# Performance work log

Measured on AMD Instinct MI355X. Metric: run time of the kernel, lower is better.

## Reference

```python
import jax, jax.numpy as jnp
import numpy as np

DIAG_MASK = 1e20  # value added on the diagonal to exclude self as negative


def setup_inputs() -> dict:
    key = jax.random.key(0)
    k1, k2, k3 = jax.random.split(key, 3)
    B, D_in, D_out = 4096, 1024, 1024
    anchor_x = jax.random.normal(k1, (B, D_in), dtype=jnp.float32)
    pos_x = jax.random.normal(k2, (B, D_in), dtype=jnp.float32)
    W = jax.random.normal(k3, (D_in, D_out), dtype=jnp.float32) * (1.0 / np.sqrt(D_in))
    b = jnp.zeros((D_out,), dtype=jnp.float32)
    return {"anchor_x": anchor_x, "pos_x": pos_x, "W": W, "b": b}


def reference(anchor_x, pos_x, W, b):
    # Encoder: simple dense projection (stand-in for the wrapped BERT encoder).
    anchor = anchor_x @ W + b          # [B, D]
    pos = pos_x @ W + b                # [B, D]

    # Pairwise squared distances dist[i,j] = ||anchor_i - pos_j||^2,
    # computed via the GEMM identity |a|^2 + |p|^2 - 2 a.p (same math as the
    # original broadcasted (a_i - p_j)^2 reduce_sum, far less memory traffic).
    a2 = jnp.sum(anchor * anchor, axis=-1, keepdims=True)       # [B, 1]
    p2 = jnp.sum(pos * pos, axis=-1, keepdims=True).T           # [1, B]
    dist = a2 + p2 - 2.0 * (anchor @ pos.T)                     # [B, B]

    B = dist.shape[0]
    mask_dist = dist + jnp.eye(B, dtype=dist.dtype) * DIAG_MASK  # mask diagonal
    indices = jnp.argmin(mask_dist, axis=-1)                     # [B] hard negatives
    neg = pos[indices]                                           # gather [B, D]

    return jnp.concatenate([anchor, pos, neg], axis=-1)          # [B, 3D]
```

## Files before the change

### kernel.cpp

```cpp
#include <hip/hip_runtime.h>


typedef short s8v __attribute__((ext_vector_type(8)));
typedef _Float16 h8v __attribute__((ext_vector_type(8)));
typedef float f4v __attribute__((ext_vector_type(4)));
typedef unsigned short u16;

#define B  4096
#define D  1024
#define OLD 3072
#define OLD16 6144
#define LDK 68

__device__ __forceinline__ u16 f2bf(float f) {
  union { float f; unsigned u; } v; v.f = f;
  unsigned r = v.u + 0x7FFFu + ((v.u >> 16) & 1u);
  return (u16)(r >> 16);
}
__device__ __forceinline__ float bf2f(u16 s) {
  union { unsigned u; float f; } v; v.u = ((unsigned)s) << 16;
  return v.f;
}

__device__ __forceinline__ void gld16(const void* g, void* l) {
  __builtin_amdgcn_global_load_lds(
      (const __attribute__((address_space(1))) unsigned int*)g,
      (__attribute__((address_space(3))) unsigned int*)l, 16, 0, 0);
}

__device__ __forceinline__ unsigned ldsaddr(const void* p) {
  const __attribute__((address_space(3))) char* lp =
      (const __attribute__((address_space(3))) char*)p;
  unsigned a;
  __builtin_memcpy(&a, &lp, 4);
  return a;
}

struct Top2 { float v1, v2; int j1, j2; };
__device__ __forceinline__ void t2_insert(Top2& t, float v, int j) {
  if (v < t.v1 || (v == t.v1 && j < t.j1)) {
    t.v2 = t.v1; t.j2 = t.j1; t.v1 = v; t.j1 = j;
  } else if (v < t.v2 || (v == t.v2 && j < t.j2)) {
    t.v2 = v; t.j2 = j;
  }
}
struct Top4 { float v[4]; int j[4]; };
__device__ __forceinline__ void t4_insert(Top4& t, float v, int j) {
  if (v < t.v[3] || (v == t.v[3] && j < t.j[3])) {
    int p = 3;
#pragma unroll
    for (int s = 0; s < 3; ++s) {
      if (p > 0 && (v < t.v[p - 1] || (v == t.v[p - 1] && j < t.j[p - 1]))) {
        t.v[p] = t.v[p - 1]; t.j[p] = t.j[p - 1]; --p;
      }
    }
    t.v[p] = v; t.j[p] = j;
  }
}

__global__ void splitT_W(const float* __restrict__ W, u16* __restrict__ WtQ) {
  __shared__ float tile[32][33];
  const int bx = blockIdx.x * 32, by = blockIdx.y * 32;
  const int tx = threadIdx.x, ty = threadIdx.y;
  for (int dy = 0; dy < 32; dy += 8)
    tile[ty + dy][tx] = W[(size_t)(by + ty + dy) * D + bx + tx];
  __syncthreads();
  for (int dy = 0; dy < 32; dy += 8) {
    const float v = tile[tx][ty + dy];
    const u16 h = f2bf(v);
    const size_t o = (size_t)(bx + ty + dy) * 2048 + by + tx;
    WtQ[o] = h;
    WtQ[o + 1024] = f2bf(v - bf2f(h));
  }
}

__global__ __launch_bounds__(256) void splitX2(
    const float* __restrict__ A, const float* __restrict__ P,
    u16* __restrict__ O16, u16* __restrict__ posXq) {
  const int r = blockIdx.x, t = threadIdx.x;
  const bool isPos = r >= B;
  const int row = isPos ? r - B : r;
  const float4 v = *(const float4*)&(isPos ? P : A)[(size_t)row * D + t * 4];
  const float vv[4] = {v.x, v.y, v.z, v.w};
  ushort4 hi, mi;
  u16* hp = &hi.x; u16* mp = &mi.x;
#pragma unroll
  for (int i = 0; i < 4; ++i) {
    hp[i] = f2bf(vv[i]);
    mp[i] = f2bf(vv[i] - bf2f(hp[i]));
  }
  if (isPos) {
    *(ushort4*)&posXq[(size_t)row * 2048 + t * 4] = hi;
    *(ushort4*)&posXq[(size_t)row * 2048 + 1024 + t * 4] = mi;
  } else {
    *(ushort4*)&O16[(size_t)row * OLD16 + 4096 + t * 4] = hi;
    *(ushort4*)&O16[(size_t)row * OLD16 + 5120 + t * 4] = mi;
  }
}

__global__ __launch_bounds__(256) void enc_mfma(
    float* out, const u16* __restrict__ posXq, const u16* __restrict__ WtQ,
    const float* __restrict__ bias, _Float16* __restrict__ Aq,
    _Float16* __restrict__ Pq) {
  __shared__ __align__(16) u16 lAh[4][128 * 32], lAm[4][128 * 32];
  __shared__ __align__(16) u16 lBh[4][128 * 32], lBm[4][128 * 32];
  const u16* O16 = (const u16*)out;
  const int tid = threadIdx.x, lane = tid & 63, wave = tid >> 6;
  const int waveM = wave >> 1, waveN = wave & 1;
  const int row16 = lane & 15, quad = lane >> 4;
  const int g = blockIdx.x + (blockIdx.y << 3);
  const int bx = (g >> 3) & 7;
  const int by = (g & 7) | ((g >> 6) << 3);
  const bool isPos = by >= 32;
  const int Mbase = (by & 31) * 128;
  const int Nbase = bx * 128;
  f4v acc[4][4] = {};
  const int slot = (quad ^ ((row16 >> 1) & 3)) * 8;

  auto STAGE = [&](int buf, int kk) {
#pragma unroll
    for (int i = 0; i < 2; ++i) {
      const int c = i * 256 + tid;
      const int row = c >> 2;
      const int col8 = ((c & 3) ^ ((row >> 1) & 3)) * 8;
      const int lo = (i * 256 + wave * 64) * 8;
      if (isPos) {
        gld16(&posXq[(size_t)(Mbase + row) * 2048 + kk + col8], &lAh[buf][lo]);
        gld16(&posXq[(size_t)(Mbase + row) * 2048 + 1024 + kk + col8], &lAm[buf][lo]);
      } else {
        gld16(&O16[(size_t)(Mbase + row) * OLD16 + 4096 + kk + col8], &lAh[buf][lo]);
        gld16(&O16[(size_t)(Mbase + row) * OLD16 + 5120 + kk + col8], &lAm[buf][lo]);
      }
      gld16(&WtQ[(size_t)(Nbase + row) * 2048 + kk + col8], &lBh[buf][lo]);
      gld16(&WtQ[(size_t)(Nbase + row) * 2048 + 1024 + kk + col8], &lBm[buf][lo]);
    }
  };

  STAGE(0, 0);
  STAGE(1, 32);
  for (int t = 0; t < 32; ++t) {
    if (t + 2 < 32) STAGE((t + 2) & 3, (t + 2) * 32);
    if (t < 30)       asm volatile("s_waitcnt vmcnt(16)" ::: "memory");
    else if (t == 30) asm volatile("s_waitcnt vmcnt(8)" ::: "memory");
    else              asm volatile("s_waitcnt vmcnt(0)" ::: "memory");
    __builtin_amdgcn_sched_barrier(0);
    __builtin_amdgcn_s_barrier();
    __builtin_amdgcn_sched_barrier(0);
    const int cur = t & 3;
    s8v ah[4], am[4], bh[4], bm[4];
#pragma unroll
    for (int mi = 0; mi < 4; ++mi) {
      const int ro = (waveM * 64 + mi * 16 + row16) * 32 + slot;
      ah[mi] = *(const s8v*)&lAh[cur][ro];
      am[mi] = *(const s8v*)&lAm[cur][ro];
    }
#pragma unroll
    for (int ni = 0; ni < 4; ++ni) {
      const int ro = (waveN * 64 + ni * 16 + row16) * 32 + slot;
      bh[ni] = *(const s8v*)&lBh[cur][ro];
      bm[ni] = *(const s8v*)&lBm[cur][ro];
    }
    __builtin_amdgcn_s_setprio(1);
#pragma unroll
    for (int mi = 0; mi < 4; ++mi)
#pragma unroll
      for (int ni = 0; ni < 4; ++ni) {
        f4v a = acc[mi][ni];
        a = __builtin_amdgcn_mfma_f32_16x16x32_bf16(ah[mi], bh[ni], a, 0, 0, 0);
        a = __builtin_amdgcn_mfma_f32_16x16x32_bf16(ah[mi], bm[ni], a, 0, 0, 0);
        a = __builtin_amdgcn_mfma_f32_16x16x32_bf16(am[mi], bh[ni], a, 0, 0, 0);
        acc[mi][ni] = a;
      }
    __builtin_amdgcn_s_setprio(0);
  }
  const int outOff = isPos ? 1024 : 0;
  _Float16* Q = isPos ? Pq : Aq;
#pragma unroll
  for (int ni = 0; ni < 4; ++ni) {
    const int col = Nbase + waveN * 64 + ni * 16 + row16;
    const float bv = bias[col];
#pragma unroll
    for (int mi = 0; mi < 4; ++mi) {
      const int rbase = Mbase + waveM * 64 + mi * 16 + quad * 4;
#pragma unroll
      for (int r = 0; r < 4; ++r) {
        const size_t row = rbase + r;
        const float v = acc[mi][ni][r] + bv;
        out[row * OLD + outOff + col] = v;
        Q[row * 1024 + col] = (_Float16)v;
      }
    }
  }
}

__global__ __launch_bounds__(256) void pnorm(float* __restrict__ o) {
  const int row = blockIdx.x, t = threadIdx.x;
  const float4 v = *(const float4*)&o[(size_t)row * OLD + D + t * 4];
  float s = v.x * v.x + v.y * v.y + v.z * v.z + v.w * v.w;
#pragma unroll
  for (int off = 32; off; off >>= 1) s += __shfl_down(s, off, 64);
  __shared__ float wsum[4];
  if ((t & 63) == 0) wsum[t >> 6] = s;
  __syncthreads();
  if (t == 0) o[(size_t)row * OLD + 2048] = wsum[0] + wsum[1] + wsum[2] + wsum[3];
}

__global__ __launch_bounds__(512, 2) void dist_mfma(
    const _Float16* __restrict__ Aq, const _Float16* __restrict__ Pq,
    float* __restrict__ o) {
  __shared__ __align__(16) u16 lA[4][256 * 32];
  __shared__ __align__(16) u16 lB[4][256 * 32];
  const int tid = threadIdx.x, lane = tid & 63, wave = tid >> 6;
  const int waveM = wave >> 2, waveN = wave & 3;
  const int row16 = lane & 15, quad = lane >> 4;
  const int Mbase = blockIdx.y * 256;
  const int Nbase = blockIdx.x * 256;
  f4v acc[8][4] = {};

  auto STAGE = [&](int buf, int kk) {
#pragma unroll
    for (int i = 0; i < 2; ++i) {
      const int c = i * 512 + tid;
      const int row = c >> 2;
      const int col8 = ((c & 3) ^ ((row >> 1) & 3)) * 8;
      u16* la = &lA[buf][(i * 512 + wave * 64) * 8];
      u16* lb = &lB[buf][(i * 512 + wave * 64) * 8];
      gld16(&Aq[(size_t)(Mbase + row) * 1024 + kk + col8], la);
      gld16(&Pq[(size_t)(Nbase + row) * 1024 + kk + col8], lb);
    }
  };

  STAGE(0, 0);
  STAGE(1, 32);
  const int slot = (quad ^ ((row16 >> 1) & 3)) * 8;
  const unsigned aoff = (unsigned)(((waveM * 128 + row16) * 32 + slot) * 2);
  const unsigned boff = (unsigned)(((waveN * 64 + row16) * 32 + slot) * 2);
  const unsigned lA0 = ldsaddr(&lA[0][0]);
  const unsigned lB0 = ldsaddr(&lB[0][0]);
  for (int t = 0; t < 32; ++t) {
    if (t + 2 < 32) STAGE((t + 2) & 3, (t + 2) * 32);
    if (t < 30)       asm volatile("s_waitcnt vmcnt(8)" ::: "memory");
    else if (t == 30) asm volatile("s_waitcnt vmcnt(4)" ::: "memory");
    else              asm volatile("s_waitcnt vmcnt(0)" ::: "memory");
    __builtin_amdgcn_sched_barrier(0);
    __builtin_amdgcn_s_barrier();
    __builtin_amdgcn_sched_barrier(0);
    const int cur = t & 3;
    const unsigned abase = lA0 + (unsigned)cur * 16384 + aoff;
    const unsigned bbase = lB0 + (unsigned)cur * 16384 + boff;
    h8v a[8], b[4];
#pragma unroll
    for (int mi = 0; mi < 8; ++mi) {
      const unsigned av = abase + (unsigned)mi * 1024;
      asm volatile("ds_read_b128 %0, %1" : "=v"(a[mi]) : "v"(av));
    }
#pragma unroll
    for (int ni = 0; ni < 4; ++ni) {
      const unsigned bv = bbase + (unsigned)ni * 1024;
      asm volatile("ds_read_b128 %0, %1" : "=v"(b[ni]) : "v"(bv));
    }
    __builtin_amdgcn_sched_barrier(0);
    asm volatile("s_waitcnt lgkmcnt(0)" ::: "memory");
    __builtin_amdgcn_sched_barrier(0);
    __builtin_amdgcn_s_setprio(1);
#pragma unroll
    for (int mi = 0; mi < 8; ++mi)
#pragma unroll
      for (int ni = 0; ni < 4; ++ni)
        acc[mi][ni] =
            __builtin_amdgcn_mfma_f32_16x16x32_f16(a[mi], b[ni], acc[mi][ni], 0, 0, 0);
    __builtin_amdgcn_s_setprio(0);
  }
  __syncthreads();

  float (*sv1)[4] = (float(*)[4])&lA[0][0];
  float (*sv2)[4] = (float(*)[4])((char*)&lA[0][0] + 4096);
  int   (*sj1)[4] = (int(*)[4])((char*)&lA[0][0] + 8192);
  int   (*sj2)[4] = (int(*)[4])((char*)&lA[0][0] + 12288);

  float p2c[4];
#pragma unroll
  for (int ni = 0; ni < 4; ++ni)
    p2c[ni] = o[(size_t)(Nbase + waveN * 64 + ni * 16 + row16) * OLD + 2048];
#pragma unroll
  for (int mi = 0; mi < 8; ++mi)
#pragma unroll
    for (int r = 0; r < 4; ++r) {
      const int rg = Mbase + waveM * 128 + mi * 16 + quad * 4 + r;
      Top2 tp; tp.v1 = 3.0e38f; tp.v2 = 3.0e38f; tp.j1 = 0; tp.j2 = 1;
#pragma unroll
      for (int ni = 0; ni < 4; ++ni) {
        const int cg = Nbase + waveN * 64 + ni * 16 + row16;
        if (cg != rg) t2_insert(tp, p2c[ni] - 2.0f * acc[mi][ni][r], cg);
      }
#pragma unroll
      for (int m = 1; m < 16; m <<= 1) {
        const float ov1 = __shfl_xor(tp.v1, m, 64);
        const int oj1 = __shfl_xor(tp.j1, m, 64);
        const float ov2 = __shfl_xor(tp.v2, m, 64);
        const int oj2 = __shfl_xor(tp.j2, m, 64);
        t2_insert(tp, ov1, oj1);
        t2_insert(tp, ov2, oj2);
      }
      if (row16 == 0) {
        const int rl = waveM * 128 + mi * 16 + quad * 4 + r;
        sv1[rl][waveN] = tp.v1; sj1[rl][waveN] = tp.j1;
        sv2[rl][waveN] = tp.v2; sj2[rl][waveN] = tp.j2;
      }
    }
  __syncthreads();
  if (tid < 256) {
    Top2 tp; tp.v1 = sv1[tid][0]; tp.j1 = sj1[tid][0];
    tp.v2 = sv2[tid][0]; tp.j2 = sj2[tid][0];
#pragma unroll
    for (int w = 1; w < 4; ++w) {
      t2_insert(tp, sv1[tid][w], sj1[tid][w]);
      t2_insert(tp, sv2[tid][w], sj2[tid][w]);
    }
    ((float4*)&o[(size_t)(Mbase + tid) * OLD + 2056])[blockIdx.x] =
        make_float4(tp.v1, __int_as_float(tp.j1), tp.v2, __int_as_float(tp.j2));
  }
}

__global__ __launch_bounds__(256) void argmin_refine(float* __restrict__ o) {
  const int i = blockIdx.x, t = threadIdx.x;
  __shared__ int gj[4];
  if (t < 64) {
    Top4 tp;
#pragma unroll
    for (int c = 0; c < 4; ++c) { tp.v[c] = 3.0e38f; tp.j[c] = 0; }
    if (t < 16) {
      const float4 p = ((const float4*)&o[(size_t)i * OLD + 2056])[t];
      t4_insert(tp, p.x, __float_as_int(p.y));
      t4_insert(tp, p.z, __float_as_int(p.w));
    }
#pragma unroll
    for (int m = 1; m < 32; m <<= 1) {
#pragma unroll
      for (int c = 0; c < 4; ++c) {
        const float ov = __shfl_xor(tp.v[c], m, 64);
        const int oj = __shfl_xor(tp.j[c], m, 64);
        t4_insert(tp, ov, oj);
      }
    }
    if (t == 0) {
#pragma unroll
      for (int c = 0; c < 4; ++c)
        gj[c] = (tp.j[c] < 0) ? 0 : (tp.j[c] > B - 1 ? B - 1 : tp.j[c]);
    }
  }
  __syncthreads();
  int jj[4];
#pragma unroll
  for (int c = 0; c < 4; ++c) jj[c] = gj[c];
  const float4 a4 = *(const float4*)&o[(size_t)i * OLD + t * 4];
  float s[4], n[4];
#pragma unroll
  for (int c = 0; c < 4; ++c) {
    const float4 q = *(const float4*)&o[(size_t)jj[c] * OLD + D + t * 4];
    s[c] = a4.x * q.x + a4.y * q.y + a4.z * q.z + a4.w * q.w;
    n[c] = q.x * q.x + q.y * q.y + q.z * q.z + q.w * q.w;
  }
#pragma unroll
  for (int off = 32; off; off >>= 1)
#pragma unroll
    for (int c = 0; c < 4; ++c) {
      s[c] += __shfl_down(s[c], off, 64);
      n[c] += __shfl_down(n[c], off, 64);
    }
  __shared__ float wsum[4][8];
  __shared__ int sjf;
  if ((t & 63) == 0)
#pragma unroll
    for (int c = 0; c < 4; ++c) {
      wsum[t >> 6][c] = s[c];
      wsum[t >> 6][4 + c] = n[c];
    }
  __syncthreads();
  if (t == 0) {
    float bd = 3.4e38f; int bj = 0x7fffffff;
#pragma unroll
    for (int c = 0; c < 4; ++c) {
      const float S = wsum[0][c] + wsum[1][c] + wsum[2][c] + wsum[3][c];
      const float N = wsum[0][4 + c] + wsum[1][4 + c] + wsum[2][4 + c] + wsum[3][4 + c];
      const float d = N - 2.0f * S;
      const int j = jj[c];
      if (d < bd || (d == bd && j < bj)) { bd = d; bj = j; }
    }
    sjf = bj;
  }
  __syncthreads();
  const int j = sjf;
  ((float4*)&o[(size_t)i * OLD + 2048])[t] = ((const float4*)&o[(size_t)j * OLD + D])[t];
}

__global__ __launch_bounds__(256) void enc_gemm(
    const float* __restrict__ X, const float* __restrict__ W,
    const float* __restrict__ bia, float* __restrict__ out, int outOff) {
  __shared__ float lA[32][LDK];
  __shared__ float lW[32][LDK];
  const int tid = threadIdx.x;
  const int Mbase = blockIdx.y * 64;
  const int Nbase = blockIdx.x * 64;
  const int ty = tid >> 4, tx = tid & 15;
  float acc[4][4] = {};
  for (int k0 = 0; k0 < D; k0 += 32) {
    __syncthreads();
#pragma unroll
    for (int h = 0; h < 2; ++h) {
      const int ch = tid + h * 256;
      const int r = ch >> 3, c4 = (ch & 7) * 4;
      const float4 a4 = *(const float4*)&X[(size_t)(Mbase + r) * D + k0 + c4];
      lA[c4 + 0][r] = a4.x; lA[c4 + 1][r] = a4.y;
      lA[c4 + 2][r] = a4.z; lA[c4 + 3][r] = a4.w;
      const int kr = ch >> 4, nc = (ch & 15) * 4;
      *(float4*)&lW[kr][nc] = *(const float4*)&W[(size_t)(k0 + kr) * D + Nbase + nc];
    }
    __syncthreads();
#pragma unroll
    for (int kk = 0; kk < 32; ++kk) {
      const float4 av = *(const float4*)&lA[kk][ty * 4];
      const float4 wv = *(const float4*)&lW[kk][tx * 4];
      acc[0][0] += av.x * wv.x; acc[0][1] += av.x * wv.y; acc[0][2] += av.x * wv.z; acc[0][3] += av.x * wv.w;
      acc[1][0] += av.y * wv.x; acc[1][1] += av.y * wv.y; acc[1][2] += av.y * wv.z; acc[1][3] += av.y * wv.w;
      acc[2][0] += av.z * wv.x; acc[2][1] += av.z * wv.y; acc[2][2] += av.z * wv.z; acc[2][3] += av.z * wv.w;
      acc[3][0] += av.w * wv.x; acc[3][1] += av.w * wv.y; acc[3][2] += av.w * wv.z; acc[3][3] += av.w * wv.w;
    }
  }
  const float4 b4 = *(const float4*)&bia[Nbase + tx * 4];
#pragma unroll
  for (int i = 0; i < 4; ++i) {
    const int row = Mbase + ty * 4 + i;
    float4 ov;
    ov.x = acc[i][0] + b4.x; ov.y = acc[i][1] + b4.y;
    ov.z = acc[i][2] + b4.z; ov.w = acc[i][3] + b4.w;
    *(float4*)&out[(size_t)row * OLD + outOff + Nbase + tx * 4] = ov;
  }
}

__global__ __launch_bounds__(256) void dist_argmin_f32(float* __restrict__ o) {
  __shared__ float lA[32][LDK];
  __shared__ float lB[32][LDK];
  const int tid = threadIdx.x;
  const int Mbase = blockIdx.y * 64, Nbase = blockIdx.x * 64;
  const int ty = tid >> 4, tx = tid & 15;
  float acc[4][4] = {};
  for (int k0 = 0; k0 < D; k0 += 32) {
    __syncthreads();
#pragma unroll
    for (int h = 0; h < 2; ++h) {
      const int ch = tid + h * 256;
      const int r = ch >> 3, c4 = (ch & 7) * 4;
      const float4 a4 = *(const float4*)&o[(size_t)(Mbase + r) * OLD + k0 + c4];
      const float4 b4 = *(const float4*)&o[(size_t)(Nbase + r) * OLD + D + k0 + c4];
      lA[c4 + 0][r] = a4.x; lA[c4 + 1][r] = a4.y;
      lA[c4 + 2][r] = a4.z; lA[c4 + 3][r] = a4.w;
      lB[c4 + 0][r] = b4.x; lB[c4 + 1][r] = b4.y;
      lB[c4 + 2][r] = b4.z; lB[c4 + 3][r] = b4.w;
    }
    __syncthreads();
#pragma unroll
    for (int kk = 0; kk < 32; ++kk) {
      const float4 av = *(const float4*)&lA[kk][ty * 4];
      const float4 bv = *(const float4*)&lB[kk][tx * 4];
      acc[0][0] += av.x * bv.x; acc[0][1] += av.x * bv.y; acc[0][2] += av.x * bv.z; acc[0][3] += av.x * bv.w;
      acc[1][0] += av.y * bv.x; acc[1][1] += av.y * bv.y; acc[1][2] += av.y * bv.z; acc[1][3] += av.y * bv.w;
      acc[2][0] += av.z * bv.x; acc[2][1] += av.z * bv.y; acc[2][2] += av.z * bv.z; acc[2][3] += av.z * bv.w;
      acc[3][0] += av.w * bv.x; acc[3][1] += av.w * bv.y; acc[3][2] += av.w * bv.z; acc[3][3] += av.w * bv.w;
    }
  }
  float colp2[4];
#pragma unroll
  for (int j = 0; j < 4; ++j)
    colp2[j] = o[(size_t)(Nbase + tx * 4 + j) * OLD + 2048];
#pragma unroll
  for (int i = 0; i < 4; ++i) {
    const int rg = Mbase + ty * 4 + i;
    float bv = 3.0e38f; int bj = 0;
#pragma unroll
    for (int j = 0; j < 4; ++j) {
      const int cg = Nbase + tx * 4 + j;
      const float d = colp2[j] - 2.0f * acc[i][j];
      if (cg != rg && d < bv) { bv = d; bj = cg; }
    }
#pragma unroll
    for (int m = 1; m < 16; m <<= 1) {
      const float ov = __shfl_xor(bv, m, 64);
      const int oj = __shfl_xor(bj, m, 64);
      if (ov < bv || (ov == bv && oj < bj)) { bv = ov; bj = oj; }
    }
    if (tx == 0)
      ((float2*)&o[(size_t)rg * OLD + 2056])[blockIdx.x] =
          make_float2(bv, __int_as_float(bj));
  }
}

__global__ __launch_bounds__(256) void argmin_final_f2(float* __restrict__ o, int nblk) {
  const int i = blockIdx.x, t = threadIdx.x;
  __shared__ int sj;
  if (t < 64) {
    float v = 3.4e38f; int j = 0x7fffffff;
    if (t < nblk) {
      const float2 p = ((const float2*)&o[(size_t)i * OLD + 2056])[t];
      v = p.x; j = __float_as_int(p.y);
    }
#pragma unroll
    for (int m = 32; m; m >>= 1) {
      const float ov = __shfl_xor(v, m, 64);
      const int oj = __shfl_xor(j, m, 64);
      if (ov < v || (ov == v && oj < j)) { v = ov; j = oj; }
    }
    if (t == 0) sj = (j < 0) ? 0 : (j > B - 1 ? B - 1 : j);
  }
  __syncthreads();
  const int j = sj;
  ((float4*)&o[(size_t)i * OLD + 2048])[t] = ((const float4*)&o[(size_t)j * OLD + D])[t];
}

extern "C" void kernel_launch(void* const* d_in, const int* in_sizes, int n_in,
                              void* d_out, int out_size, void* d_ws, size_t ws_size,
                              hipStream_t stream) {
  const float* anchor_x = (const float*)d_in[0];
  const float* pos_x    = (const float*)d_in[1];
  const float* W        = (const float*)d_in[2];
  const float* b        = (const float*)d_in[3];
  float* out = (float*)d_out;
  char* ws = (char*)d_ws;
  const size_t MB = 1024 * 1024;

  if (ws_size >= 36 * MB) {
    _Float16* Aq = (_Float16*)(ws);
    _Float16* Pq = (_Float16*)(ws + 8 * MB);
    u16* WtQ     = (u16*)(ws + 16 * MB);
    u16* posXq   = (u16*)(ws + 20 * MB);
    splitT_W<<<dim3(32, 32), dim3(32, 8), 0, stream>>>(W, WtQ);
    splitX2<<<2 * B, 256, 0, stream>>>(anchor_x, pos_x, (u16*)out, posXq);
    enc_mfma<<<dim3(8, 64), 256, 0, stream>>>(out, posXq, WtQ, b, Aq, Pq);
    pnorm<<<B, 256, 0, stream>>>(out);
    dist_mfma<<<dim3(16, 16), 512, 0, stream>>>(Aq, Pq, out);
    argmin_refine<<<B, 256, 0, stream>>>(out);
  } else {
    enc_gemm<<<dim3(16, 64), 256, 0, stream>>>(anchor_x, W, b, out, 0);
    enc_gemm<<<dim3(16, 64), 256, 0, stream>>>(pos_x,    W, b, out, 1024);
    pnorm<<<B, 256, 0, stream>>>(out);
    dist_argmin_f32<<<dim3(64, 64), 256, 0, stream>>>(out);
    argmin_final_f2<<<B, 256, 0, stream>>>(out, 64);
  }
}
```

Measured before the change: 294.8 us.

## Merge split kernels and fuse positive-norm computation into encoder epilogue

Combines the W transpose-split and input split kernels into one launch. It also computes the squared norms of the positive embeddings inside the encoder GEMM epilogue using shuffles and atomicAdd into a workspace buffer, which removes the separate pnorm pass. This saves two kernel launches and one read of the positive rows. In exchange it adds atomics and a zero-initialization that must finish before the encoder runs. The workspace threshold rises by 1 MB, and argmin_refine may still read the old location, a consistency risk.

```diff
diff --git a/kernel.cpp b/kernel.cpp
--- a/kernel.cpp
+++ b/kernel.cpp
@@ -58,50 +58,53 @@
   }
 }
 
-__global__ void splitT_W(const float* __restrict__ W, u16* __restrict__ WtQ) {
+__global__ __launch_bounds__(256) void split_all(
+    const float* __restrict__ A, const float* __restrict__ P,
+    const float* __restrict__ W, u16* __restrict__ O16,
+    u16* __restrict__ posXq, u16* __restrict__ WtQ, float* __restrict__ p2) {
   __shared__ float tile[32][33];
-  const int bx = blockIdx.x * 32, by = blockIdx.y * 32;
-  const int tx = threadIdx.x, ty = threadIdx.y;
-  for (int dy = 0; dy < 32; dy += 8)
-    tile[ty + dy][tx] = W[(size_t)(by + ty + dy) * D + bx + tx];
-  __syncthreads();
-  for (int dy = 0; dy < 32; dy += 8) {
-    const float v = tile[tx][ty + dy];
-    const u16 h = f2bf(v);
-    const size_t o = (size_t)(bx + ty + dy) * 2048 + by + tx;
-    WtQ[o] = h;
-    WtQ[o + 1024] = f2bf(v - bf2f(h));
-  }
-}
-
-__global__ __launch_bounds__(256) void splitX2(
-    const float* __restrict__ A, const float* __restrict__ P,
-    u16* __restrict__ O16, u16* __restrict__ posXq) {
-  const int r = blockIdx.x, t = threadIdx.x;
-  const bool isPos = r >= B;
-  const int row = isPos ? r - B : r;
-  const float4 v = *(const float4*)&(isPos ? P : A)[(size_t)row * D + t * 4];
-  const float vv[4] = {v.x, v.y, v.z, v.w};
-  ushort4 hi, mi;
-  u16* hp = &hi.x; u16* mp = &mi.x;
-#pragma unroll
-  for (int i = 0; i < 4; ++i) {
-    hp[i] = f2bf(vv[i]);
-    mp[i] = f2bf(vv[i] - bf2f(hp[i]));
-  }
-  if (isPos) {
-    *(ushort4*)&posXq[(size_t)row * 2048 + t * 4] = hi;
-    *(ushort4*)&posXq[(size_t)row * 2048 + 1024 + t * 4] = mi;
+  const int bb = blockIdx.x, tid = threadIdx.x;
+  if (bb < 2 * B) {
+    const bool isPos = bb >= B;
+    const int row = isPos ? bb - B : bb;
+    const float4 v = *(const float4*)&(isPos ? P : A)[(size_t)row * D + tid * 4];
+    const float vv[4] = {v.x, v.y, v.z, v.w};
+    ushort4 hi, mi;
+    u16* hp = &hi.x; u16* mp = &mi.x;
+#pragma unroll
+    for (int i = 0; i < 4; ++i) {
+      hp[i] = f2bf(vv[i]);
+      mp[i] = f2bf(vv[i] - bf2f(hp[i]));
+    }
+    if (isPos) {
+      *(ushort4*)&posXq[(size_t)row * 2048 + tid * 4] = hi;
+      *(ushort4*)&posXq[(size_t)row * 2048 + 1024 + tid * 4] = mi;
+      if (tid == 0) p2[row] = 0.0f;
+    } else {
+      *(ushort4*)&O16[(size_t)row * OLD16 + 4096 + tid * 4] = hi;
+      *(ushort4*)&O16[(size_t)row * OLD16 + 5120 + tid * 4] = mi;
+    }
   } else {
-    *(ushort4*)&O16[(size_t)row * OLD16 + 4096 + t * 4] = hi;
-    *(ushort4*)&O16[(size_t)row * OLD16 + 5120 + t * 4] = mi;
+    const int b2 = bb - 2 * B;
+    const int bx = (b2 & 31) * 32, by = (b2 >> 5) * 32;
+    const int tx = tid & 31, ty = tid >> 5;
+    for (int dy = 0; dy < 32; dy += 8)
+      tile[ty + dy][tx] = W[(size_t)(by + ty + dy) * D + bx + tx];
+    __syncthreads();
+    for (int dy = 0; dy < 32; dy += 8) {
+      const float v = tile[tx][ty + dy];
+      const u16 h = f2bf(v);
+      const size_t o = (size_t)(bx + ty + dy) * 2048 + by + tx;
+      WtQ[o] = h;
+      WtQ[o + 1024] = f2bf(v - bf2f(h));
+    }
   }
 }
 
 __global__ __launch_bounds__(256) void enc_mfma(
     float* out, const u16* __restrict__ posXq, const u16* __restrict__ WtQ,
     const float* __restrict__ bias, _Float16* __restrict__ Aq,
-    _Float16* __restrict__ Pq) {
+    _Float16* __restrict__ Pq, float* __restrict__ p2) {
   __shared__ __align__(16) u16 lAh[4][128 * 32], lAm[4][128 * 32];
   __shared__ __align__(16) u16 lBh[4][128 * 32], lBm[4][128 * 32];
   const u16* O16 = (const u16*)out;
@@ -175,19 +178,31 @@
   }
   const int outOff = isPos ? 1024 : 0;
   _Float16* Q = isPos ? Pq : Aq;
-#pragma unroll
-  for (int ni = 0; ni < 4; ++ni) {
-    const int col = Nbase + waveN * 64 + ni * 16 + row16;
-    const float bv = bias[col];
-#pragma unroll
-    for (int mi = 0; mi < 4; ++mi) {
-      const int rbase = Mbase + waveM * 64 + mi * 16 + quad * 4;
-#pragma unroll
-      for (int r = 0; r < 4; ++r) {
-        const size_t row = rbase + r;
-        const float v = acc[mi][ni][r] + bv;
+  float bv4[4];
+#pragma unroll
+  for (int ni = 0; ni < 4; ++ni)
+    bv4[ni] = bias[Nbase + waveN * 64 + ni * 16 + row16];
+#pragma unroll
+  for (int mi = 0; mi < 4; ++mi) {
+    const int rbase = Mbase + waveM * 64 + mi * 16 + quad * 4;
+#pragma unroll
+    for (int r = 0; r < 4; ++r) {
+      const size_t row = rbase + r;
+      float ss = 0.0f;
+#pragma unroll
+      for (int ni = 0; ni < 4; ++ni) {
+        const int col = Nbase + waveN * 64 + ni * 16 + row16;
+        const float v = acc[mi][ni][r] + bv4[ni];
         out[row * OLD + outOff + col] = v;
         Q[row * 1024 + col] = (_Float16)v;
+        ss += v * v;
+      }
+      if (isPos) {
+        ss += __shfl_xor(ss, 1, 64);
+        ss += __shfl_xor(ss, 2, 64);
+        ss += __shfl_xor(ss, 4, 64);
+        ss += __shfl_xor(ss, 8, 64);
+        if (row16 == 0) atomicAdd(&p2[row], ss);
       }
     }
   }
@@ -207,7 +222,7 @@
 
 __global__ __launch_bounds__(512, 2) void dist_mfma(
     const _Float16* __restrict__ Aq, const _Float16* __restrict__ Pq,
-    float* __restrict__ o) {
+    const float* __restrict__ p2, float* __restrict__ o) {
   __shared__ __align__(16) u16 lA[4][256 * 32];
   __shared__ __align__(16) u16 lB[4][256 * 32];
   const int tid = threadIdx.x, lane = tid & 63, wave = tid >> 6;
@@ -281,7 +296,7 @@
   float p2c[4];
 #pragma unroll
   for (int ni = 0; ni < 4; ++ni)
-    p2c[ni] = o[(size_t)(Nbase + waveN * 64 + ni * 16 + row16) * OLD + 2048];
+    p2c[ni] = p2[Nbase + waveN * 64 + ni * 16 + row16];
 #pragma unroll
   for (int mi = 0; mi < 8; ++mi)
 #pragma unroll
@@ -528,16 +543,16 @@
   char* ws = (char*)d_ws;
   const size_t MB = 1024 * 1024;
 
-  if (ws_size >= 36 * MB) {
+  if (ws_size >= 37 * MB) {
     _Float16* Aq = (_Float16*)(ws);
     _Float16* Pq = (_Float16*)(ws + 8 * MB);
     u16* WtQ     = (u16*)(ws + 16 * MB);
     u16* posXq   = (u16*)(ws + 20 * MB);
-    splitT_W<<<dim3(32, 32), dim3(32, 8), 0, stream>>>(W, WtQ);
-    splitX2<<<2 * B, 256, 0, stream>>>(anchor_x, pos_x, (u16*)out, posXq);
-    enc_mfma<<<dim3(8, 64), 256, 0, stream>>>(out, posXq, WtQ, b, Aq, Pq);
-    pnorm<<<B, 256, 0, stream>>>(out);
-    dist_mfma<<<dim3(16, 16), 512, 0, stream>>>(Aq, Pq, out);
+    float* p2    = (float*)(ws + 36 * MB);
+    split_all<<<2 * B + 1024, 256, 0, stream>>>(anchor_x, pos_x, W,
+                                                (u16*)out, posXq, WtQ, p2);
+    enc_mfma<<<dim3(8, 64), 256, 0, stream>>>(out, posXq, WtQ, b, Aq, Pq, p2);
+    dist_mfma<<<dim3(16, 16), 512, 0, stream>>>(Aq, Pq, p2, out);
     argmin_refine<<<B, 256, 0, stream>>>(out);
   } else {
     enc_gemm<<<dim3(16, 64), 256, 0, stream>>>(anchor_x, W, b, out, 0);
```

Measured after the change: 298.9 us. About the same (+1.4%).
